# Kernel tuning notes

Measured on AMD Instinct MI355X. Metric: run time of the kernel, lower is better.

The kernel has to match this reference:

```python
import jax, jax.numpy as jnp
import numpy as np

N, E, T, NORB, H, C = 10000, 100000, 200000, 9, 128, 64


def _normalize(v, eps=1e-12):
    # F.normalize: v / max(||v||_2, eps) along last dim
    n = jnp.linalg.norm(v, axis=-1, keepdims=True)
    return v / jnp.maximum(n, eps)


def setup_inputs() -> dict:
    key = jax.random.key(0)
    ks = jax.random.split(key, 24)
    p = lambda i, shape, scale=0.05: jax.random.normal(ks[i], shape, jnp.float32) * scale
    return {
        "x": jax.random.normal(ks[0], (N, H), jnp.float32),
        "cji": jax.random.normal(ks[1], (E, NORB, C), jnp.float32),
        "cutoff_w": jax.random.uniform(ks[2], (E,), jnp.float32),
        "rb": jax.random.normal(ks[3], (E, NORB), jnp.float32),
        "shb": jax.random.normal(ks[4], (T, NORB), jnp.float32),
        "idx_i": jax.random.randint(ks[5], (E,), 0, N),
        "idx_j": jax.random.randint(ks[6], (E,), 0, N),
        "tri_idx_k": jax.random.randint(ks[7], (T,), 0, N),
        "edge_idx_kj": jax.random.randint(ks[8], (T,), 0, E),
        "edge_idx_ji": jax.random.randint(ks[9], (T,), 0, E),
        "w_node": p(10, (H, 2 * C)),
        "b_node": jnp.zeros((2 * C,), jnp.float32),
        "w_c1": p(11, (C, C)),  # coeffs_dim == C here
        "w_c2": p(12, (C, C)),
        "w_t1": p(13, (C, C)),
        "b_t1": jnp.zeros((C,), jnp.float32),
        "w_t2": p(14, (C, C)),
        "b_t2": jnp.zeros((C,), jnp.float32),
        "w_basis": p(15, (C, C)),
        "w_n1": p(16, (2 * C, C)),
        "b_n1": jnp.zeros((C,), jnp.float32),
        "w_n2": p(17, (C, C)),
        "b_n2": jnp.zeros((C,), jnp.float32),
        "w_out": p(18, (C, H)),
    }


def reference(x, cji, cutoff_w, rb, shb, idx_i, idx_j, tri_idx_k, edge_idx_kj,
              edge_idx_ji, w_node, b_node, w_c1, w_c2, w_t1, b_t1, w_t2, b_t2,
              w_basis, w_n1, b_n1, w_n2, b_n2, w_out):
    silu = jax.nn.silu
    x_before = x
    # node_weight -> chunk into (x, xk), each (N, C)
    h = x @ w_node + b_node
    x1, xk = h[:, :C], h[:, C:]
    # f_coeffs: two bias-free Dense + SiLU, per (E, n_orb) position
    cji = silu(silu(cji @ w_c1) @ w_c2)  # (E, NORB, C)
    # cutoff weighting on radial basis
    rb = rb * cutoff_w[:, None]  # (E, NORB)
    # triplet gather + contraction over orbital axis d
    ckj = cji[edge_idx_kj]  # (T, NORB, C)
    three_body_orbs = jnp.einsum("td,tdh->th", rb[edge_idx_kj] * shb, ckj)  # (T, C)
    three_body_orbs = _normalize(three_body_orbs)
    xk_g = jax.nn.sigmoid(xk[tri_idx_k])  # (T, C)
    three_body_w = three_body_orbs * xk_g
    # scatter-sum triplets -> edges, then f_three MLP
    agg = jax.ops.segment_sum(three_body_w, edge_idx_ji, num_segments=E)  # (E, C)
    three_body_w = silu(silu(agg @ w_t1 + b_t1) @ w_t2 + b_t2)  # (E, C)
    cji = cji + cji * three_body_w[:, None, :]  # (E, NORB, C)
    # LCAO weights: contract radial basis with coefficients
    lcao_w = jnp.einsum("ed,edh->eh", rb, cji)  # (E, C)
    lcao_w = _normalize(lcao_w) @ w_basis
    # f_node on gathered endpoint features
    pair = jnp.concatenate([x1[idx_i], x1[idx_j]], axis=-1)  # (E, 2C)
    fnode = silu(silu(pair @ w_n1 + b_n1) @ w_n2 + b_n2)  # (E, C)
    msg = lcao_w * fnode
    out = x_before + jax.ops.segment_sum(msg, idx_i, num_segments=N) @ w_out
    return out
```

## Files before the change

kernel.cpp:

```cpp
#include <hip/hip_runtime.h>
#include <math.h>

typedef __attribute__((ext_vector_type(8))) short bf16x8;
typedef __attribute__((ext_vector_type(4))) float f32x4;
typedef __attribute__((ext_vector_type(4))) unsigned int uint32x4;
typedef unsigned int uint32;
typedef unsigned short ushort;

#define N_NODES 10000
#define E_EDGES 100000
#define T_TRI   200000
#define NORB    9
#define H_DIM   128
#define C_DIM   64
#define LSTR    68

__device__ __forceinline__ ushort f2b_rtne(float f) {
  uint32 u = __float_as_uint(f);
  u += 0x7FFFu + ((u >> 16) & 1u);
  return (ushort)(u >> 16);
}
__device__ __forceinline__ uint32 rtne2(float a, float b) {
  uint32 ua = __float_as_uint(a), ub = __float_as_uint(b);
  ua += 0x7FFFu + ((ua >> 16) & 1u);
  ub += 0x7FFFu + ((ub >> 16) & 1u);
  return (ua >> 16) | (ub & 0xFFFF0000u);
}
__device__ __forceinline__ uint32 trunc2(float a, float b) {
  return (__float_as_uint(a) >> 16) | (__float_as_uint(b) & 0xFFFF0000u);
}
__device__ __forceinline__ float b2f(ushort u) {
  return __uint_as_float(((uint32)u) << 16);
}
__device__ __forceinline__ float blo(uint32 u) {
  return __uint_as_float(u << 16);
}
__device__ __forceinline__ float bhi(uint32 u) {
  return __uint_as_float(u & 0xFFFF0000u);
}
__device__ __forceinline__ float silu_f(float x) {
  return x * __builtin_amdgcn_rcpf(1.0f + __expf(-x));
}
__device__ __forceinline__ float sigmoid_f(float x) {
  return __builtin_amdgcn_rcpf(1.0f + __expf(-x));
}
__device__ __forceinline__ float rl(float v, int k) {
  return __uint_as_float(__builtin_amdgcn_readlane(__float_as_uint(v), k));
}
__device__ __forceinline__ f32x4 mfma16(bf16x8 a, bf16x8 b, f32x4 c) {
  return __builtin_amdgcn_mfma_f32_16x16x32_bf16(a, b, c, 0, 0, 0);
}
__device__ __forceinline__ void atom_pk_bf16(ushort* addr, uint32 val) {
  asm volatile("global_atomic_pk_add_bf16 %0, %1, off"
               :: "v"(addr), "v"(val) : "memory");
}
#define LDS_FENCE() asm volatile("s_waitcnt lgkmcnt(0)" ::: "memory")

__device__ __forceinline__ bf16x8 pack8(const float* p) {
  f32x4 v0 = *(const f32x4*)p;
  f32x4 v1 = *(const f32x4*)(p + 4);
  uint32x4 u;
  u[0] = trunc2(v0[0], v0[1]);
  u[1] = trunc2(v0[2], v0[3]);
  u[2] = trunc2(v1[0], v1[1]);
  u[3] = trunc2(v1[2], v1[3]);
  return __builtin_bit_cast(bf16x8, u);
}
__device__ __forceinline__ bf16x8 pack8v(f32x4 v0, f32x4 v1) {
  uint32x4 u;
  u[0] = trunc2(v0[0], v0[1]);
  u[1] = trunc2(v0[2], v0[3]);
  u[2] = trunc2(v1[0], v1[1]);
  u[3] = trunc2(v1[2], v1[3]);
  return __builtin_bit_cast(bf16x8, u);
}
__device__ __forceinline__ bf16x8 bfrag_w(const float* W, int kt, int ct, int lane) {
  const float* p = W + (size_t)(kt * 32 + ((lane >> 4) * 8)) * 64 + ct * 16 + (lane & 15);
  bf16x8 r;
#pragma unroll
  for (int b = 0; b < 8; ++b) r[b] = (short)f2b_rtne(p[(size_t)b * 64]);
  return r;
}

__global__ __launch_bounds__(128) void k_node_mlp(
    const float* __restrict__ x, const float* __restrict__ w_node,
    const float* __restrict__ b_node, ushort* __restrict__ x1b,
    ushort* __restrict__ sigxkb) {
  __shared__ float xs[H_DIM];
  int n = blockIdx.x;
  int c = threadIdx.x;
  xs[c] = x[(size_t)n * H_DIM + c];
  __syncthreads();
  float acc = b_node[c];
#pragma unroll 8
  for (int k = 0; k < H_DIM; ++k)
    acc = fmaf(xs[k], w_node[k * H_DIM + c], acc);
  if (c < C_DIM)
    x1b[(size_t)n * C_DIM + c] = f2b_rtne(acc);
  else
    sigxkb[(size_t)n * C_DIM + (c - C_DIM)] = f2b_rtne(sigmoid_f(acc));
}

__global__ __launch_bounds__(256) void k_cji_mlp_mfma(
    const float* __restrict__ cji, const float* __restrict__ w_c1,
    const float* __restrict__ w_c2, ushort* __restrict__ cji2) {
  __shared__ __align__(16) float lds_all[4][16 * LSTR];
  int lane = threadIdx.x & 63;
  float* lds = lds_all[threadIdx.x >> 6];
  int wid = (blockIdx.x * 256 + (int)threadIdx.x) >> 6;
  int nw = (gridDim.x * 256) >> 6;
  bf16x8 w1f[2][4], w2f[2][4];
#pragma unroll
  for (int kt = 0; kt < 2; ++kt)
#pragma unroll
    for (int ct = 0; ct < 4; ++ct) {
      w1f[kt][ct] = bfrag_w(w_c1, kt, ct, lane);
      w2f[kt][ct] = bfrag_w(w_c2, kt, ct, lane);
    }
  const int nstrips = (E_EDGES * NORB) / 16;
  int l15 = lane & 15, g = lane >> 4;
  int wrow = g * 4, wcol = l15;
  f32x4 z = {0.f, 0.f, 0.f, 0.f};
  int s = wid;
  f32x4 nv0, nv1, nv2, nv3;
  if (s < nstrips) {
    const float* ap = cji + (size_t)(s * 16 + l15) * 64 + g * 8;
    nv0 = *(const f32x4*)ap;
    nv1 = *(const f32x4*)(ap + 4);
    nv2 = *(const f32x4*)(ap + 32);
    nv3 = *(const f32x4*)(ap + 36);
  }
  while (s < nstrips) {
    f32x4 c0 = nv0, c1 = nv1, c2 = nv2, c3 = nv3;
    int sn = s + nw;
    if (sn < nstrips) {
      const float* np = cji + (size_t)(sn * 16 + l15) * 64 + g * 8;
      nv0 = *(const f32x4*)np;
      nv1 = *(const f32x4*)(np + 4);
      nv2 = *(const f32x4*)(np + 32);
      nv3 = *(const f32x4*)(np + 36);
    }
    bf16x8 a0 = pack8v(c0, c1), a1 = pack8v(c2, c3);
#pragma unroll
    for (int ct = 0; ct < 4; ++ct) {
      f32x4 acc = mfma16(a0, w1f[0][ct], z);
      acc = mfma16(a1, w1f[1][ct], acc);
#pragma unroll
      for (int r = 0; r < 4; ++r)
        lds[(wrow + r) * LSTR + ct * 16 + wcol] = silu_f(acc[r]);
    }
    LDS_FENCE();
    bf16x8 t0 = pack8(lds + l15 * LSTR + g * 8);
    bf16x8 t1 = pack8(lds + l15 * LSTR + 32 + g * 8);
#pragma unroll
    for (int ct = 0; ct < 4; ++ct) {
      f32x4 acc = mfma16(t0, w2f[0][ct], z);
      acc = mfma16(t1, w2f[1][ct], acc);
#pragma unroll
      for (int r = 0; r < 4; ++r)
        lds[(wrow + r) * LSTR + ct * 16 + wcol] = silu_f(acc[r]);
    }
    LDS_FENCE();
    const float* lp = lds + l15 * LSTR + g * 16;
    f32x4 v0 = *(const f32x4*)lp;
    f32x4 v1 = *(const f32x4*)(lp + 4);
    f32x4 v2 = *(const f32x4*)(lp + 8);
    f32x4 v3 = *(const f32x4*)(lp + 12);
    uint32x4 o0, o1;
    o0[0] = rtne2(v0[0], v0[1]); o0[1] = rtne2(v0[2], v0[3]);
    o0[2] = rtne2(v1[0], v1[1]); o0[3] = rtne2(v1[2], v1[3]);
    o1[0] = rtne2(v2[0], v2[1]); o1[1] = rtne2(v2[2], v2[3]);
    o1[2] = rtne2(v3[0], v3[1]); o1[3] = rtne2(v3[2], v3[3]);
    uint32x4* dst = (uint32x4*)(cji2 + (size_t)(s * 16 + l15) * 64 + g * 16);
    dst[0] = o0;
    dst[1] = o1;
    s = sn;
  }
}

__global__ __launch_bounds__(256) void k_triplet_pk(
    const ushort* __restrict__ cji2, const float* __restrict__ rb,
    const float* __restrict__ cutoff_w, const float* __restrict__ shb,
    const int* __restrict__ tri_idx_k, const int* __restrict__ edge_idx_kj,
    const int* __restrict__ edge_idx_ji, const ushort* __restrict__ sigxkb,
    ushort* __restrict__ aggb) {
  int lane = threadIdx.x & 63;
  int half = lane >> 5;
  int l = lane & 31;
  int wid = (blockIdx.x * 256 + (int)threadIdx.x) >> 6;
  int nw = (gridDim.x * 256) >> 6;
  const uint32* c2 = (const uint32*)cji2;
  const uint32* sx = (const uint32*)sigxkb;
  for (int tb = wid; tb < T_TRI / 2; tb += nw) {
    int t = tb * 2 + half;
    int e = edge_idx_kj[t];
    float cw = cutoff_w[e];
    const uint32* crow = c2 + (size_t)e * (NORB * 32);
    float a0 = 0.f, a1 = 0.f;
#pragma unroll
    for (int d = 0; d < NORB; ++d) {
      uint32 u = crow[d * 32 + l];
      float coeff = rb[e * NORB + d] * cw * shb[t * NORB + d];
      a0 = fmaf(coeff, blo(u), a0);
      a1 = fmaf(coeff, bhi(u), a1);
    }
    float ss = a0 * a0 + a1 * a1;
#pragma unroll
    for (int m = 16; m >= 1; m >>= 1) ss += __shfl_xor(ss, m, 64);
    float scale = __builtin_amdgcn_rsqf(fmaxf(ss, 1e-30f));
    int kn = tri_idx_k[t];
    uint32 gx = sx[(size_t)kn * 32 + l];
    float v0 = a0 * scale * blo(gx);
    float v1 = a1 * scale * bhi(gx);
    int ej = edge_idx_ji[t];
    atom_pk_bf16(aggb + (size_t)ej * C_DIM + 2 * l, rtne2(v0, v1));
  }
}

__global__ __launch_bounds__(256) void k_tbw_lcao(
    const ushort* __restrict__ aggb, const float* __restrict__ w_t1,
    const float* __restrict__ b_t1, const float* __restrict__ w_t2,
    const float* __restrict__ b_t2, const ushort* __restrict__ cji2,
    const float* __restrict__ rb, const float* __restrict__ cutoff_w,
    const float* __restrict__ w_basis, float* __restrict__ lcao) {
  __shared__ __align__(16) float lds_all[4][16 * LSTR];
  int lane = threadIdx.x & 63;
  float* lds = lds_all[threadIdx.x >> 6];
  int wid = (blockIdx.x * 256 + (int)threadIdx.x) >> 6;
  int nw = (gridDim.x * 256) >> 6;
  bf16x8 wt1[2][4], wt2[2][4], wb[2][4];
  float bt1[4], bt2[4];
  int l15 = lane & 15, g = lane >> 4;
#pragma unroll
  for (int ct = 0; ct < 4; ++ct) {
    bt1[ct] = b_t1[ct * 16 + l15];
    bt2[ct] = b_t2[ct * 16 + l15];
#pragma unroll
    for (int kt = 0; kt < 2; ++kt) {
      wt1[kt][ct] = bfrag_w(w_t1, kt, ct, lane);
      wt2[kt][ct] = bfrag_w(w_t2, kt, ct, lane);
      wb[kt][ct] = bfrag_w(w_basis, kt, ct, lane);
    }
  }
  const int nstrips = E_EDGES / 16;
  int wrow = g * 4, wcol = l15;
  f32x4 z = {0.f, 0.f, 0.f, 0.f};
  for (int s = wid; s < nstrips; s += nw) {
    const uint32x4* ap = (const uint32x4*)(aggb + (size_t)(s * 16 + l15) * 64 + g * 8);
    bf16x8 a0 = __builtin_bit_cast(bf16x8, ap[0]);
    bf16x8 a1 = __builtin_bit_cast(bf16x8, ap[2]);
#pragma unroll
    for (int ct = 0; ct < 4; ++ct) {
      f32x4 acc = mfma16(a0, wt1[0][ct], z);
      acc = mfma16(a1, wt1[1][ct], acc);
#pragma unroll
      for (int r = 0; r < 4; ++r)
        lds[(wrow + r) * LSTR + ct * 16 + wcol] = silu_f(acc[r] + bt1[ct]);
    }
    LDS_FENCE();
    bf16x8 t0 = pack8(lds + l15 * LSTR + g * 8);
    bf16x8 t1 = pack8(lds + l15 * LSTR + 32 + g * 8);
    LDS_FENCE();
#pragma unroll
    for (int ct = 0; ct < 4; ++ct) {
      f32x4 acc = mfma16(t0, wt2[0][ct], z);
      acc = mfma16(t1, wt2[1][ct], acc);
#pragma unroll
      for (int r = 0; r < 4; ++r)
        lds[(wrow + r) * LSTR + ct * 16 + wcol] = silu_f(acc[r] + bt2[ct]);
    }
    LDS_FENCE();
    for (int ee = 0; ee < 16; ++ee) {
      int e = s * 16 + ee;
      float cw = cutoff_w[e];
      const ushort* crow = cji2 + (size_t)e * (NORB * C_DIM);
      float acc = 0.f;
#pragma unroll
      for (int d = 0; d < NORB; ++d)
        acc = fmaf(rb[e * NORB + d] * cw, b2f(crow[d * C_DIM + lane]), acc);
      acc *= (1.0f + lds[ee * LSTR + lane]);
      float ss = acc * acc;
#pragma unroll
      for (int m = 32; m >= 1; m >>= 1) ss += __shfl_xor(ss, m, 64);
      float scale = __builtin_amdgcn_rsqf(fmaxf(ss, 1e-30f));
      lds[ee * LSTR + lane] = acc * scale;
    }
    LDS_FENCE();
    bf16x8 n0 = pack8(lds + l15 * LSTR + g * 8);
    bf16x8 n1 = pack8(lds + l15 * LSTR + 32 + g * 8);
    LDS_FENCE();
    f32x4 o[4];
#pragma unroll
    for (int ct = 0; ct < 4; ++ct) {
      o[ct] = mfma16(n0, wb[0][ct], z);
      o[ct] = mfma16(n1, wb[1][ct], o[ct]);
#pragma unroll
      for (int r = 0; r < 4; ++r)
        lds[(wrow + r) * LSTR + ct * 16 + wcol] = o[ct][r];
    }
    LDS_FENCE();
    const float* lp = lds + l15 * LSTR + g * 16;
    f32x4* dst = (f32x4*)(lcao + (size_t)(s * 16 + l15) * 64 + g * 16);
    dst[0] = *(const f32x4*)lp;
    dst[1] = *(const f32x4*)(lp + 4);
    dst[2] = *(const f32x4*)(lp + 8);
    dst[3] = *(const f32x4*)(lp + 12);
  }
}

__global__ __launch_bounds__(256) void k_msg_mfma(
    const ushort* __restrict__ x1b, const int* __restrict__ idx_i,
    const int* __restrict__ idx_j, const float* __restrict__ w_n1,
    const float* __restrict__ b_n1, const float* __restrict__ w_n2,
    const float* __restrict__ b_n2, const float* __restrict__ lcao,
    float* __restrict__ nodeagg) {
  __shared__ __align__(16) float lds_all[4][16 * LSTR];
  int lane = threadIdx.x & 63;
  float* lds = lds_all[threadIdx.x >> 6];
  int wid = (blockIdx.x * 256 + (int)threadIdx.x) >> 6;
  int nw = (gridDim.x * 256) >> 6;
  bf16x8 wn1f[4][4], wn2f[2][4];
  float bn1[4], bn2[4];
  int l15 = lane & 15, g = lane >> 4;
#pragma unroll
  for (int ct = 0; ct < 4; ++ct) {
    bn1[ct] = b_n1[ct * 16 + l15];
    bn2[ct] = b_n2[ct * 16 + l15];
#pragma unroll
    for (int kt = 0; kt < 4; ++kt) wn1f[kt][ct] = bfrag_w(w_n1, kt, ct, lane);
#pragma unroll
    for (int kt = 0; kt < 2; ++kt) wn2f[kt][ct] = bfrag_w(w_n2, kt, ct, lane);
  }
  const int nstrips = E_EDGES / 16;
  int wrow = g * 4, wcol = l15;
  f32x4 z = {0.f, 0.f, 0.f, 0.f};
  for (int s = wid; s < nstrips; s += nw) {
    int er = s * 16 + l15;
    int ii = idx_i[er], jj = idx_j[er];
    const uint32x4* pi = (const uint32x4*)(x1b + (size_t)ii * 64 + g * 8);
    const uint32x4* pj = (const uint32x4*)(x1b + (size_t)jj * 64 + g * 8);
    bf16x8 a0 = __builtin_bit_cast(bf16x8, pi[0]);
    bf16x8 a1 = __builtin_bit_cast(bf16x8, pi[2]);
    bf16x8 a2 = __builtin_bit_cast(bf16x8, pj[0]);
    bf16x8 a3 = __builtin_bit_cast(bf16x8, pj[2]);
#pragma unroll
    for (int ct = 0; ct < 4; ++ct) {
      f32x4 acc = mfma16(a0, wn1f[0][ct], z);
      acc = mfma16(a1, wn1f[1][ct], acc);
      acc = mfma16(a2, wn1f[2][ct], acc);
      acc = mfma16(a3, wn1f[3][ct], acc);
#pragma unroll
      for (int r = 0; r < 4; ++r)
        lds[(wrow + r) * LSTR + ct * 16 + wcol] = silu_f(acc[r] + bn1[ct]);
    }
    LDS_FENCE();
    bf16x8 t0 = pack8(lds + l15 * LSTR + g * 8);
    bf16x8 t1 = pack8(lds + l15 * LSTR + 32 + g * 8);
    f32x4 acc2[4];
#pragma unroll
    for (int ct = 0; ct < 4; ++ct) {
      acc2[ct] = mfma16(t0, wn2f[0][ct], z);
      acc2[ct] = mfma16(t1, wn2f[1][ct], acc2[ct]);
    }
#pragma unroll
    for (int r = 0; r < 4; ++r) {
      int ge = s * 16 + wrow + r;
      int ni = idx_i[ge];
#pragma unroll
      for (int ct = 0; ct < 4; ++ct) {
        float f = silu_f(acc2[ct][r] + bn2[ct]);
        float m = lcao[(size_t)ge * 64 + ct * 16 + l15] * f;
        atomicAdd(&nodeagg[(size_t)ni * 64 + ct * 16 + l15], m);
      }
    }
  }
}

__global__ __launch_bounds__(256) void k_out(
    const float* __restrict__ x, const float* __restrict__ nodeagg,
    const float* __restrict__ w_out, float* __restrict__ out) {
  int lane = threadIdx.x & 63;
  int wid = (blockIdx.x * 256 + (int)threadIdx.x) >> 6;
  int nw = (gridDim.x * 256) >> 6;
  float wo0[64], wo1[64];
#pragma unroll
  for (int k = 0; k < 64; ++k) wo0[k] = w_out[k * H_DIM + lane];
#pragma unroll
  for (int k = 0; k < 64; ++k) wo1[k] = w_out[k * H_DIM + 64 + lane];
  for (int n = wid; n < N_NODES; n += nw) {
    float v = nodeagg[(size_t)n * 64 + lane];
    float a0 = 0.f, a1 = 0.f;
#pragma unroll
    for (int k = 0; k < 64; ++k) {
      float a = rl(v, k);
      a0 = fmaf(a, wo0[k], a0);
      a1 = fmaf(a, wo1[k], a1);
    }
    out[(size_t)n * H_DIM + lane] = x[(size_t)n * H_DIM + lane] + a0;
    out[(size_t)n * H_DIM + 64 + lane] = x[(size_t)n * H_DIM + 64 + lane] + a1;
  }
}

extern "C" void kernel_launch(void* const* d_in, const int* in_sizes, int n_in,
                              void* d_out, int out_size, void* d_ws, size_t ws_size,
                              hipStream_t stream) {
  const float* x         = (const float*)d_in[0];
  const float* cji       = (const float*)d_in[1];
  const float* cutoff_w  = (const float*)d_in[2];
  const float* rb        = (const float*)d_in[3];
  const float* shb       = (const float*)d_in[4];
  const int*   idx_i     = (const int*)d_in[5];
  const int*   idx_j     = (const int*)d_in[6];
  const int*   tri_idx_k = (const int*)d_in[7];
  const int*   e_kj      = (const int*)d_in[8];
  const int*   e_ji      = (const int*)d_in[9];
  const float* w_node    = (const float*)d_in[10];
  const float* b_node    = (const float*)d_in[11];
  const float* w_c1      = (const float*)d_in[12];
  const float* w_c2      = (const float*)d_in[13];
  const float* w_t1      = (const float*)d_in[14];
  const float* b_t1      = (const float*)d_in[15];
  const float* w_t2      = (const float*)d_in[16];
  const float* b_t2      = (const float*)d_in[17];
  const float* w_basis   = (const float*)d_in[18];
  const float* w_n1      = (const float*)d_in[19];
  const float* b_n1      = (const float*)d_in[20];
  const float* w_n2      = (const float*)d_in[21];
  const float* b_n2      = (const float*)d_in[22];
  const float* w_out     = (const float*)d_in[23];
  float* out = (float*)d_out;

  char* ws = (char*)d_ws;
  ushort* x1b    = (ushort*)(ws + 0);
  ushort* sigxkb = (ushort*)(ws + 1280000);
  ushort* cji2   = (ushort*)(ws + 2560000);
  ushort* aggb   = (ushort*)(ws + 117760000);
  float*  lcao   = (float*)(ws + 143360000);
  float*  nodeagg= (float*)(ws + 168960000);

  (void)hipMemsetAsync(aggb, 0, (size_t)6400000 * sizeof(ushort), stream);
  (void)hipMemsetAsync(nodeagg, 0, (size_t)640000 * sizeof(float), stream);

  k_node_mlp<<<N_NODES, 128, 0, stream>>>(x, w_node, b_node, x1b, sigxkb);
  k_cji_mlp_mfma<<<2048, 256, 0, stream>>>(cji, w_c1, w_c2, cji2);
  k_triplet_pk<<<2048, 256, 0, stream>>>(cji2, rb, cutoff_w, shb, tri_idx_k,
                                         e_kj, e_ji, sigxkb, aggb);
  k_tbw_lcao<<<1024, 256, 0, stream>>>(aggb, w_t1, b_t1, w_t2, b_t2, cji2,
                                       rb, cutoff_w, w_basis, lcao);
  k_msg_mfma<<<1024, 256, 0, stream>>>(x1b, idx_i, idx_j, w_n1, b_n1, w_n2,
                                       b_n2, lcao, nodeagg);
  k_out<<<256, 256, 0, stream>>>(x, nodeagg, w_out, out);
}
```

Measured before the change: 257.6 us.

## Process strip pairs in cji MLP and use packed bf16 node-aggregation atomics

The cji MLP kernel now handles two 16-row strips per loop iteration with separate LDS buffers, interleaving their MFMA chains in place of the previous register prefetch of the next strip. The message kernel pairs adjacent lanes through a shuffle and issues packed bf16 atomic adds into a bf16 node accumulator, halving the atomic operations and the accumulator footprint. The output kernel reads the bf16 accumulator. This trades accumulation precision for fewer atomics, and removing the explicit prefetch may expose load latency.

Measured after the change: 261.4 us. Within noise of the previous version (+1.5%).

```diff
diff --git a/kernel.cpp b/kernel.cpp
--- a/kernel.cpp
+++ b/kernel.cpp
@@ -59,14 +59,6 @@
 __device__ __forceinline__ bf16x8 pack8(const float* p) {
   f32x4 v0 = *(const f32x4*)p;
   f32x4 v1 = *(const f32x4*)(p + 4);
-  uint32x4 u;
-  u[0] = trunc2(v0[0], v0[1]);
-  u[1] = trunc2(v0[2], v0[3]);
-  u[2] = trunc2(v1[0], v1[1]);
-  u[3] = trunc2(v1[2], v1[3]);
-  return __builtin_bit_cast(bf16x8, u);
-}
-__device__ __forceinline__ bf16x8 pack8v(f32x4 v0, f32x4 v1) {
   uint32x4 u;
   u[0] = trunc2(v0[0], v0[1]);
   u[1] = trunc2(v0[2], v0[3]);
@@ -104,9 +96,10 @@
 __global__ __launch_bounds__(256) void k_cji_mlp_mfma(
     const float* __restrict__ cji, const float* __restrict__ w_c1,
     const float* __restrict__ w_c2, ushort* __restrict__ cji2) {
-  __shared__ __align__(16) float lds_all[4][16 * LSTR];
+  __shared__ __align__(16) float lds_all[4][2][16 * LSTR];
   int lane = threadIdx.x & 63;
-  float* lds = lds_all[threadIdx.x >> 6];
+  float* ldsA = lds_all[threadIdx.x >> 6][0];
+  float* ldsB = lds_all[threadIdx.x >> 6][1];
   int wid = (blockIdx.x * 256 + (int)threadIdx.x) >> 6;
   int nw = (gridDim.x * 256) >> 6;
   bf16x8 w1f[2][4], w2f[2][4];
@@ -117,64 +110,63 @@
       w1f[kt][ct] = bfrag_w(w_c1, kt, ct, lane);
       w2f[kt][ct] = bfrag_w(w_c2, kt, ct, lane);
     }
-  const int nstrips = (E_EDGES * NORB) / 16;
+  const int npairs = (E_EDGES * NORB) / 32;
   int l15 = lane & 15, g = lane >> 4;
   int wrow = g * 4, wcol = l15;
   f32x4 z = {0.f, 0.f, 0.f, 0.f};
-  int s = wid;
-  f32x4 nv0, nv1, nv2, nv3;
-  if (s < nstrips) {
-    const float* ap = cji + (size_t)(s * 16 + l15) * 64 + g * 8;
-    nv0 = *(const f32x4*)ap;
-    nv1 = *(const f32x4*)(ap + 4);
-    nv2 = *(const f32x4*)(ap + 32);
-    nv3 = *(const f32x4*)(ap + 36);
-  }
-  while (s < nstrips) {
-    f32x4 c0 = nv0, c1 = nv1, c2 = nv2, c3 = nv3;
-    int sn = s + nw;
-    if (sn < nstrips) {
-      const float* np = cji + (size_t)(sn * 16 + l15) * 64 + g * 8;
-      nv0 = *(const f32x4*)np;
-      nv1 = *(const f32x4*)(np + 4);
-      nv2 = *(const f32x4*)(np + 32);
-      nv3 = *(const f32x4*)(np + 36);
-    }
-    bf16x8 a0 = pack8v(c0, c1), a1 = pack8v(c2, c3);
-#pragma unroll
-    for (int ct = 0; ct < 4; ++ct) {
-      f32x4 acc = mfma16(a0, w1f[0][ct], z);
-      acc = mfma16(a1, w1f[1][ct], acc);
-#pragma unroll
-      for (int r = 0; r < 4; ++r)
-        lds[(wrow + r) * LSTR + ct * 16 + wcol] = silu_f(acc[r]);
-    }
-    LDS_FENCE();
-    bf16x8 t0 = pack8(lds + l15 * LSTR + g * 8);
-    bf16x8 t1 = pack8(lds + l15 * LSTR + 32 + g * 8);
-#pragma unroll
-    for (int ct = 0; ct < 4; ++ct) {
-      f32x4 acc = mfma16(t0, w2f[0][ct], z);
-      acc = mfma16(t1, w2f[1][ct], acc);
-#pragma unroll
-      for (int r = 0; r < 4; ++r)
-        lds[(wrow + r) * LSTR + ct * 16 + wcol] = silu_f(acc[r]);
-    }
-    LDS_FENCE();
-    const float* lp = lds + l15 * LSTR + g * 16;
-    f32x4 v0 = *(const f32x4*)lp;
-    f32x4 v1 = *(const f32x4*)(lp + 4);
-    f32x4 v2 = *(const f32x4*)(lp + 8);
-    f32x4 v3 = *(const f32x4*)(lp + 12);
-    uint32x4 o0, o1;
-    o0[0] = rtne2(v0[0], v0[1]); o0[1] = rtne2(v0[2], v0[3]);
-    o0[2] = rtne2(v1[0], v1[1]); o0[3] = rtne2(v1[2], v1[3]);
-    o1[0] = rtne2(v2[0], v2[1]); o1[1] = rtne2(v2[2], v2[3]);
-    o1[2] = rtne2(v3[0], v3[1]); o1[3] = rtne2(v3[2], v3[3]);
-    uint32x4* dst = (uint32x4*)(cji2 + (size_t)(s * 16 + l15) * 64 + g * 16);
-    dst[0] = o0;
-    dst[1] = o1;
-    s = sn;
+  for (int sp = wid; sp < npairs; sp += nw) {
+    int s0 = sp * 2, s1 = sp * 2 + 1;
+    const float* apA = cji + (size_t)(s0 * 16 + l15) * 64 + g * 8;
+    const float* apB = cji + (size_t)(s1 * 16 + l15) * 64 + g * 8;
+    bf16x8 a0 = pack8(apA), a1 = pack8(apA + 32);
+    bf16x8 b0 = pack8(apB), b1 = pack8(apB + 32);
+#pragma unroll
+    for (int ct = 0; ct < 4; ++ct) {
+      f32x4 accA = mfma16(a0, w1f[0][ct], z);
+      accA = mfma16(a1, w1f[1][ct], accA);
+      f32x4 accB = mfma16(b0, w1f[0][ct], z);
+      accB = mfma16(b1, w1f[1][ct], accB);
+#pragma unroll
+      for (int r = 0; r < 4; ++r) {
+        ldsA[(wrow + r) * LSTR + ct * 16 + wcol] = silu_f(accA[r]);
+        ldsB[(wrow + r) * LSTR + ct * 16 + wcol] = silu_f(accB[r]);
+      }
+    }
+    LDS_FENCE();
+    bf16x8 tA0 = pack8(ldsA + l15 * LSTR + g * 8);
+    bf16x8 tA1 = pack8(ldsA + l15 * LSTR + 32 + g * 8);
+    bf16x8 tB0 = pack8(ldsB + l15 * LSTR + g * 8);
+    bf16x8 tB1 = pack8(ldsB + l15 * LSTR + 32 + g * 8);
+#pragma unroll
+    for (int ct = 0; ct < 4; ++ct) {
+      f32x4 accA = mfma16(tA0, w2f[0][ct], z);
+      accA = mfma16(tA1, w2f[1][ct], accA);
+      f32x4 accB = mfma16(tB0, w2f[0][ct], z);
+      accB = mfma16(tB1, w2f[1][ct], accB);
+#pragma unroll
+      for (int r = 0; r < 4; ++r) {
+        ldsA[(wrow + r) * LSTR + ct * 16 + wcol] = silu_f(accA[r]);
+        ldsB[(wrow + r) * LSTR + ct * 16 + wcol] = silu_f(accB[r]);
+      }
+    }
+    LDS_FENCE();
+#pragma unroll
+    for (int q = 0; q < 2; ++q) {
+      const float* lp = (q ? ldsB : ldsA) + l15 * LSTR + g * 16;
+      int s = q ? s1 : s0;
+      f32x4 v0 = *(const f32x4*)lp;
+      f32x4 v1 = *(const f32x4*)(lp + 4);
+      f32x4 v2 = *(const f32x4*)(lp + 8);
+      f32x4 v3 = *(const f32x4*)(lp + 12);
+      uint32x4 o0, o1;
+      o0[0] = rtne2(v0[0], v0[1]); o0[1] = rtne2(v0[2], v0[3]);
+      o0[2] = rtne2(v1[0], v1[1]); o0[3] = rtne2(v1[2], v1[3]);
+      o1[0] = rtne2(v2[0], v2[1]); o1[1] = rtne2(v2[2], v2[3]);
+      o1[2] = rtne2(v3[0], v3[1]); o1[3] = rtne2(v3[2], v3[3]);
+      uint32x4* dst = (uint32x4*)(cji2 + (size_t)(s * 16 + l15) * 64 + g * 16);
+      dst[0] = o0;
+      dst[1] = o1;
+    }
   }
 }
 
@@ -313,7 +305,7 @@
     const int* __restrict__ idx_j, const float* __restrict__ w_n1,
     const float* __restrict__ b_n1, const float* __restrict__ w_n2,
     const float* __restrict__ b_n2, const float* __restrict__ lcao,
-    float* __restrict__ nodeagg) {
+    ushort* __restrict__ nodeaggb) {
   __shared__ __align__(16) float lds_all[4][16 * LSTR];
   int lane = threadIdx.x & 63;
   float* lds = lds_all[threadIdx.x >> 6];
@@ -370,14 +362,16 @@
       for (int ct = 0; ct < 4; ++ct) {
         float f = silu_f(acc2[ct][r] + bn2[ct]);
         float m = lcao[(size_t)ge * 64 + ct * 16 + l15] * f;
-        atomicAdd(&nodeagg[(size_t)ni * 64 + ct * 16 + l15], m);
+        float mn = __shfl_xor(m, 1, 64);
+        if (!(l15 & 1))
+          atom_pk_bf16(nodeaggb + (size_t)ni * 64 + ct * 16 + l15, rtne2(m, mn));
       }
     }
   }
 }
 
 __global__ __launch_bounds__(256) void k_out(
-    const float* __restrict__ x, const float* __restrict__ nodeagg,
+    const float* __restrict__ x, const ushort* __restrict__ nodeaggb,
     const float* __restrict__ w_out, float* __restrict__ out) {
   int lane = threadIdx.x & 63;
   int wid = (blockIdx.x * 256 + (int)threadIdx.x) >> 6;
@@ -388,7 +382,7 @@
 #pragma unroll
   for (int k = 0; k < 64; ++k) wo1[k] = w_out[k * H_DIM + 64 + lane];
   for (int n = wid; n < N_NODES; n += nw) {
-    float v = nodeagg[(size_t)n * 64 + lane];
+    float v = b2f(nodeaggb[(size_t)n * 64 + lane]);
     float a0 = 0.f, a1 = 0.f;
 #pragma unroll
     for (int k = 0; k < 64; ++k) {
@@ -431,15 +425,15 @@
   float* out = (float*)d_out;
 
   char* ws = (char*)d_ws;
-  ushort* x1b    = (ushort*)(ws + 0);
-  ushort* sigxkb = (ushort*)(ws + 1280000);
-  ushort* cji2   = (ushort*)(ws + 2560000);
-  ushort* aggb   = (ushort*)(ws + 117760000);
-  float*  lcao   = (float*)(ws + 143360000);
-  float*  nodeagg= (float*)(ws + 168960000);
+  ushort* x1b     = (ushort*)(ws + 0);
+  ushort* sigxkb  = (ushort*)(ws + 1280000);
+  ushort* cji2    = (ushort*)(ws + 2560000);
+  ushort* aggb    = (ushort*)(ws + 117760000);
+  float*  lcao    = (float*)(ws + 143360000);
+  ushort* nodeaggb= (ushort*)(ws + 168960000);
 
   (void)hipMemsetAsync(aggb, 0, (size_t)6400000 * sizeof(ushort), stream);
-  (void)hipMemsetAsync(nodeagg, 0, (size_t)640000 * sizeof(float), stream);
+  (void)hipMemsetAsync(nodeaggb, 0, (size_t)640000 * sizeof(ushort), stream);
 
   k_node_mlp<<<N_NODES, 128, 0, stream>>>(x, w_node, b_node, x1b, sigxkb);
   k_cji_mlp_mfma<<<2048, 256, 0, stream>>>(cji, w_c1, w_c2, cji2);
@@ -448,6 +442,6 @@
   k_tbw_lcao<<<1024, 256, 0, stream>>>(aggb, w_t1, b_t1, w_t2, b_t2, cji2,
                                        rb, cutoff_w, w_basis, lcao);
   k_msg_mfma<<<1024, 256, 0, stream>>>(x1b, idx_i, idx_j, w_n1, b_n1, w_n2,
-                                       b_n2, lcao, nodeagg);
-  k_out<<<256, 256, 0, stream>>>(x, nodeagg, w_out, out);
-}
+                                       b_n2, lcao, nodeaggb);
+  k_out<<<256, 256, 0, stream>>>(x, nodeaggb, w_out, out);
+}
```
